# Kernel optimization log

Hardware: AMD Instinct MI355X
Metric: run time of the kernel (lower is better)

The kernel has to match this reference:

```python
import jax, jax.numpy as jnp
import numpy as np

N = 6144          # num utterances (graph nodes)
D = 128           # utt_embed_size
WIN = 10          # att_window_size
NUM_SPK = 8
N_EMO = 7


def _init(key, shape):
    fan_in = shape[0]
    return jax.random.normal(key, shape, dtype=jnp.float32) * (1.0 / np.sqrt(fan_in))


def setup_inputs() -> dict:
    key = jax.random.key(0)
    ks = jax.random.split(key, 20)
    inp = {
        "x": jax.random.normal(ks[0], (N, D), dtype=jnp.float32),
        "speakers": jax.random.randint(ks[1], (N,), 0, NUM_SPK, dtype=jnp.int32),
        # layer-1 relation GCN weights (pred / suc / same / diff)
        "W_pred1": _init(ks[2], (D, D)),
        "W_suc1": _init(ks[3], (D, D)),
        "W_same1": _init(ks[4], (D, D)),
        "W_diff1": _init(ks[5], (D, D)),
        # layer-2 relation GCN weights
        "W_pred2": _init(ks[6], (D, D)),
        "W_suc2": _init(ks[7], (D, D)),
        "W_same2": _init(ks[8], (D, D)),
        "W_diff2": _init(ks[9], (D, D)),
        "w_aggr_1": _init(ks[10], (D, D)),
        "w_aggr_2": _init(ks[11], (D, D)),
        "w_e1": _init(ks[12], (2 * D, D)),
        "b_e1": jnp.zeros((D,), dtype=jnp.float32),
        "w_e2": _init(ks[13], (D, N_EMO)),
        "b_e2": jnp.zeros((N_EMO,), dtype=jnp.float32),
        "w_s": _init(ks[14], (2 * D, N_EMO)),
        "b_s": jnp.zeros((N_EMO,), dtype=jnp.float32),
    }
    return inp


def reference(x, speakers, W_pred1, W_suc1, W_same1, W_diff1,
              W_pred2, W_suc2, W_same2, W_diff2,
              w_aggr_1, w_aggr_2, w_e1, b_e1, w_e2, b_e2, w_s, b_s):
    n = x.shape[0]
    idx = jnp.arange(n)
    # windowed dot-product attention; entries outside the window stay 0.0
    # BEFORE the softmax (faithful to the torch code: zeros, not -inf)
    band = jnp.abs(idx[:, None] - idx[None, :]) <= WIN
    scores = jnp.where(band, x @ x.T, 0.0)            # [N, N]
    attn = jax.nn.softmax(scores, axis=1)
    # relation masks
    same = (speakers[:, None] == speakers[None, :]).astype(x.dtype)
    pred = (idx[None, :] >= idx[:, None]).astype(x.dtype)   # triu incl diag
    suc = 1.0 - pred                                          # strict lower tri
    adjs = (same * pred * attn,        # same-speaker, predecessor
            same * suc * attn,         # same-speaker, successor
            (1.0 - same) * pred * attn,  # diff-speaker, predecessor
            (1.0 - same) * suc * attn)   # diff-speaker, successor

    def gcn(h, Ws):  # sum_k adj_k @ (h @ W_k)
        return sum(a @ (h @ w) for a, w in zip(adjs, Ws))

    d = jnp.diagonal(attn)[:, None]   # self-attention scale
    h1 = jax.nn.relu(gcn(x, (W_pred1, W_suc1, W_same1, W_diff1))
                     + (x @ w_aggr_1) * d)
    h2 = jax.nn.relu(gcn(h1, (W_pred2, W_suc2, W_same2, W_diff2))
                     + (h1 @ w_aggr_2) * d)
    h = jnp.concatenate([h2, x], axis=1)              # [N, 2D]
    emotion = jax.nn.relu(h @ w_e1 + b_e1) @ w_e2 + b_e2   # [N, 7]
    sentiment = h @ w_s + b_s                               # [N, 7]
    return emotion, sentiment
```

## Files before the change

### kernel.cpp

```cpp
#include <hip/hip_runtime.h>
#include <hip/hip_bf16.h>


#define NN   6144
#define DD   128
#define WINW 10
#define YST  168
#define TAB_OFF 27456
#define SS_OFF  33088
#define SM_BYTES 35904
#define NBLK 768
#define WS_W1T 0
#define WS_W2T 163840
#define WS_WE1 327680
#define WS_WE2 393216
#define WS_WST 397312
#define WS_H1  405504
#define WS_H2  1978368
#define BAR_OFF 3551232
#define BAR_STRIDE 16384
#define BAR_BYTES (3 * BAR_STRIDE)

typedef unsigned short u16;
typedef __attribute__((ext_vector_type(8))) short bf16x8;
typedef __attribute__((ext_vector_type(4))) float f32x4;

__device__ __forceinline__ float b2f(u16 u) {
    return __uint_as_float(((unsigned int)u) << 16);
}
__device__ __forceinline__ u16 f2b(float f) {
    __hip_bfloat16 h = __float2bfloat16(f);
    return *reinterpret_cast<u16*>(&h);
}
__device__ __forceinline__ bf16x8 cvt8(const float* p) {
    float4 u = *reinterpret_cast<const float4*>(p);
    float4 v = *reinterpret_cast<const float4*>(p + 4);
    bf16x8 r;
    r[0] = (short)f2b(u.x); r[1] = (short)f2b(u.y);
    r[2] = (short)f2b(u.z); r[3] = (short)f2b(u.w);
    r[4] = (short)f2b(v.x); r[5] = (short)f2b(v.y);
    r[6] = (short)f2b(v.z); r[7] = (short)f2b(v.w);
    return r;
}
__device__ __forceinline__ void st_agent_u32(unsigned* p, unsigned v) {
    __hip_atomic_store(p, v, __ATOMIC_RELAXED, __HIP_MEMORY_SCOPE_AGENT);
}
__device__ __forceinline__ unsigned ld_agent_u32(const unsigned* p) {
    return __hip_atomic_load(p, __ATOMIC_RELAXED, __HIP_MEMORY_SCOPE_AGENT);
}
__device__ __forceinline__ const float* sel5(int r,
    const float* a0, const float* a1, const float* a2,
    const float* a3, const float* a4) {
    return r == 0 ? a0 : r == 1 ? a1 : r == 2 ? a2 : r == 3 ? a3 : a4;
}

__device__ __forceinline__ void grid_barrier(char* barbase, int b) {
    __syncthreads();
    if (threadIdx.x == 0) {
        char* base = barbase + b * BAR_STRIDE;
        unsigned g = blockIdx.x >> 5;
        unsigned* gctr  = (unsigned*)(base + g * 128);
        unsigned* rctr  = (unsigned*)(base + 4096);
        unsigned* gflag = (unsigned*)(base + 8192 + g * 128);
        unsigned* rflag = (unsigned*)(base + 12288);
        unsigned r = __hip_atomic_fetch_add(gctr, 1u, __ATOMIC_RELAXED,
                                            __HIP_MEMORY_SCOPE_AGENT);
        if (r == 31u) {
            unsigned rr = __hip_atomic_fetch_add(rctr, 1u, __ATOMIC_RELAXED,
                                                 __HIP_MEMORY_SCOPE_AGENT);
            if (rr == 23u) {
                st_agent_u32(rflag, 1u);
            } else {
                while (ld_agent_u32(rflag) == 0u)
                    __builtin_amdgcn_s_sleep(1);
            }
            st_agent_u32(gflag, 1u);
        } else {
            while (ld_agent_u32(gflag) == 0u)
                __builtin_amdgcn_s_sleep(1);
        }
    }
    __syncthreads();
    __builtin_amdgcn_sched_barrier(0);
}

__device__ __forceinline__ void layer_tile(
    const float* __restrict__ x, const u16* __restrict__ Ab16,
    const u16* __restrict__ BT, const int* __restrict__ spk,
    u16* __restrict__ hout, int first_layer, int hb, int bm,
    char* smraw, int tid)
{
    u16*   Ys  = (u16*)smraw;
    float* Xs  = (float*)smraw;
    int2*  tab = (int2*)(smraw + TAB_OFF);
    float* Ss  = (float*)(smraw + SS_OFF);
    const int wave = tid >> 6, lane = tid & 63;
    const int lm = lane & 15, quad = lane >> 4;
    const int wm = wave >> 1, wn = wave & 1;

    bf16x8 afr[2][4];

    if (first_layer) {
        #pragma unroll
        for (int it = 0; it < 7; ++it) {
            int f = tid + it * 256;
            if (f < 52 * 32) {
                int s = f >> 5, c = f & 31;
                int g = min(max(bm - WINW + s, 0), NN - 1);
                *reinterpret_cast<float4*>(&Xs[s * 132 + c * 4]) =
                    *reinterpret_cast<const float4*>(&x[(size_t)g * DD + c * 4]);
            }
        }
        __syncthreads();

        #pragma unroll
        for (int rr = 0; rr < 3; ++rr) {
            int p = tid + rr * 256;
            if (p < 672) {
                int il = p / 21, o = p - il * 21;
                int jg = bm + il - WINW + o;
                float sv = -1e30f;
                if (jg >= 0 && jg < NN) {
                    const float* xr = &Xs[(il + WINW) * 132];
                    const float* jr = &Xs[(il + o) * 132];
                    float a0 = 0.f, a1 = 0.f, a2 = 0.f, a3 = 0.f;
                    #pragma unroll 8
                    for (int k4 = 0; k4 < 32; ++k4) {
                        float4 a = *reinterpret_cast<const float4*>(xr + k4 * 4);
                        float4 b = *reinterpret_cast<const float4*>(jr + k4 * 4);
                        a0 = fmaf(a.x, b.x, a0); a1 = fmaf(a.y, b.y, a1);
                        a2 = fmaf(a.z, b.z, a2); a3 = fmaf(a.w, b.w, a3);
                    }
                    sv = (a0 + a1) + (a2 + a3);
                }
                Ss[il * 22 + o] = sv;
            }
        }
        __syncthreads();

        if (tid < 32) {
            int il = tid, i = bm + il;
            float m = 0.f;
            #pragma unroll
            for (int o = 0; o < 21; ++o) {
                float s = Ss[il * 22 + o];
                if (s > -1e29f) m = fmaxf(m, s);
            }
            int lo = i - WINW; if (lo < 0) lo = 0;
            int hi = i + WINW; if (hi > NN - 1) hi = NN - 1;
            float Z = (float)(NN - (hi - lo + 1)) * __expf(-m);
            float ev[21];
            #pragma unroll
            for (int o = 0; o < 21; ++o) {
                float s = Ss[il * 22 + o];
                ev[o] = (s > -1e29f) ? __expf(s - m) : 0.f;
                Z += ev[o];
            }
            float rz = 1.f / Z;
            #pragma unroll
            for (int o = 0; o < 21; ++o) Ss[il * 22 + o] = ev[o] * rz;
        }
        __syncthreads();

        #pragma unroll
        for (int rr = 0; rr < 3; ++rr) {
            int p = tid + rr * 256;
            if (p < 704) {
                int il = p / 22, e = p - il * 22;
                int i  = bm + il;
                int si = spk[i];
                float w; int off;
                if (e < 21) {
                    int j = i - WINW + e;
                    bool valid = (j >= 0) && (j < NN);
                    int jc  = valid ? j : i;
                    int sel = (spk[jc] == si) ? ((j >= i) ? 0 : 1)
                                              : ((j >= i) ? 2 : 3);
                    w   = valid ? Ss[il * 22 + e] : 0.f;
                    off = valid ? (il + e) * YST + sel * 32 : 0;
                } else {
                    w   = Ss[il * 22 + WINW];
                    off = (il + WINW) * YST + 4 * 32;
                }
                tab[p] = make_int2(__float_as_int(w), off);
            }
        }

        #pragma unroll
        for (int mt = 0; mt < 2; ++mt) {
            int rl = min((wm * 2 + mt) * 16 + lm, 51);
            #pragma unroll
            for (int s = 0; s < 4; ++s)
                afr[mt][s] = cvt8(&Xs[rl * 132 + s * 32 + quad * 8]);
        }
        __syncthreads();
    } else {
        #pragma unroll
        for (int mt = 0; mt < 2; ++mt) {
            int gr = min(max(bm - WINW + (wm * 2 + mt) * 16 + lm, 0), NN - 1);
            #pragma unroll
            for (int s = 0; s < 4; ++s)
                afr[mt][s] = *reinterpret_cast<const bf16x8*>(
                    Ab16 + (size_t)gr * DD + s * 32 + quad * 8);
        }
    }

    f32x4 acc[2][5];
    #pragma unroll
    for (int mt = 0; mt < 2; ++mt)
        #pragma unroll
        for (int n = 0; n < 5; ++n) acc[mt][n] = {0.f, 0.f, 0.f, 0.f};

    #pragma unroll
    for (int np = 0; np < 5; ++np) {
        int nt = wn * 5 + np;
        int gn = (nt >> 1) * 128 + hb * 32 + (nt & 1) * 16 + lm;
        #pragma unroll
        for (int s = 0; s < 4; ++s) {
            bf16x8 b = *reinterpret_cast<const bf16x8*>(
                BT + (size_t)gn * DD + s * 32 + quad * 8);
            acc[0][np] = __builtin_amdgcn_mfma_f32_16x16x32_bf16(afr[0][s], b, acc[0][np], 0, 0, 0);
            acc[1][np] = __builtin_amdgcn_mfma_f32_16x16x32_bf16(afr[1][s], b, acc[1][np], 0, 0, 0);
        }
    }
    #pragma unroll
    for (int mt = 0; mt < 2; ++mt)
        #pragma unroll
        for (int np = 0; np < 5; ++np) {
            int nt = wn * 5 + np;
            #pragma unroll
            for (int r = 0; r < 4; ++r) {
                int lr = (wm * 2 + mt) * 16 + quad * 4 + r;
                if (lr < 52) Ys[lr * YST + nt * 16 + lm] = f2b(acc[mt][np][r]);
            }
        }
    __syncthreads();

    const int c0 = (tid & 15) * 2;
    const int rg = tid >> 4;
    #pragma unroll
    for (int rr = 0; rr < 2; ++rr) {
        int il = rg * 2 + rr;
        float a0 = 0.f, a1 = 0.f;
        const int2* tp = &tab[il * 22];
        #pragma unroll
        for (int e = 0; e < 22; ++e) {
            int2 t = tp[e];
            float w = __int_as_float(t.x);
            unsigned y2 = *reinterpret_cast<const unsigned*>(Ys + t.y + c0);
            a0 = fmaf(w, b2f((u16)(y2 & 0xffff)), a0);
            a1 = fmaf(w, b2f((u16)(y2 >> 16)), a1);
        }
        int i = bm + il;
        unsigned pk = ((unsigned)f2b(fmaxf(a1, 0.f)) << 16) | f2b(fmaxf(a0, 0.f));
        st_agent_u32(reinterpret_cast<unsigned*>(
            &hout[(size_t)i * DD + hb * 32 + c0]), pk);
    }
}

__global__ __launch_bounds__(256, 4) void fused_kernel(
    const float* __restrict__ x, const int* __restrict__ spk,
    const float* __restrict__ p0, const float* __restrict__ p1,
    const float* __restrict__ p2, const float* __restrict__ p3,
    const float* __restrict__ p4,
    const float* __restrict__ q0, const float* __restrict__ q1,
    const float* __restrict__ q2, const float* __restrict__ q3,
    const float* __restrict__ q4,
    const float* __restrict__ we1, const float* __restrict__ be1,
    const float* __restrict__ we2, const float* __restrict__ be2,
    const float* __restrict__ wss, const float* __restrict__ bss,
    float* __restrict__ out, char* __restrict__ ws)
{
    u16*   W1T   = (u16*)(ws + WS_W1T);
    u16*   W2T   = (u16*)(ws + WS_W2T);
    u16*   We1T  = (u16*)(ws + WS_WE1);
    u16*   we2T  = (u16*)(ws + WS_WE2);
    u16*   wsT   = (u16*)(ws + WS_WST);
    u16*   h1b   = (u16*)(ws + WS_H1);
    u16*   h2b   = (u16*)(ws + WS_H2);
    char*  bar   = ws + BAR_OFF;

    __shared__ __align__(16) char smraw[SM_BYTES];
    const int bid = blockIdx.x;
    const int tid = threadIdx.x;

    if (bid < 160) {
        unsigned* W1T32 = (unsigned*)W1T;
        unsigned* W2T32 = (unsigned*)W2T;
        int idx = bid * 256 + tid;
        int c = idx & 127, rk = idx >> 7;
        int r = rk >> 6, k2 = rk & 63, k = k2 * 2;
        const float* s1 = sel5(r, p0, p1, p2, p3, p4);
        const float* s2 = sel5(r, q0, q1, q2, q3, q4);
        unsigned v1 = (unsigned)f2b(s1[k * 128 + c]) |
                      ((unsigned)f2b(s1[(k + 1) * 128 + c]) << 16);
        unsigned v2 = (unsigned)f2b(s2[k * 128 + c]) |
                      ((unsigned)f2b(s2[(k + 1) * 128 + c]) << 16);
        int U = (r * 128 + c) * 64 + k2;
        st_agent_u32(&W1T32[U], v1);
        st_agent_u32(&W2T32[U], v2);
    } else if (bid < 192) {
        unsigned* We1T32 = (unsigned*)We1T;
        #pragma unroll
        for (int it = 0; it < 2; ++it) {
            int idx = (bid - 160) * 256 + tid + it * 8192;
            int n = idx & 127, k2 = idx >> 7, k = k2 * 2;
            unsigned v = (unsigned)f2b(we1[k * 128 + n]) |
                         ((unsigned)f2b(we1[(k + 1) * 128 + n]) << 16);
            st_agent_u32(&We1T32[n * 128 + k2], v);
        }
    } else if (bid == 192) {
        unsigned* we2T32 = (unsigned*)we2T;
        #pragma unroll
        for (int it = 0; it < 4; ++it) {
            int U = tid + it * 256;
            int n = U >> 6, kh = U & 63, k = kh * 2;
            float lo = n < 7 ? we2[k * 7 + n] : 0.f;
            float hi = n < 7 ? we2[(k + 1) * 7 + n] : 0.f;
            st_agent_u32(&we2T32[U],
                         (unsigned)f2b(lo) | ((unsigned)f2b(hi) << 16));
        }
    } else if (bid == 193) {
        unsigned* wsT32 = (unsigned*)wsT;
        #pragma unroll
        for (int it = 0; it < 8; ++it) {
            int U = tid + it * 256;
            int n = U >> 7, kh = U & 127, k = kh * 2;
            float lo = n < 7 ? wss[k * 7 + n] : 0.f;
            float hi = n < 7 ? wss[(k + 1) * 7 + n] : 0.f;
            st_agent_u32(&wsT32[U],
                         (unsigned)f2b(lo) | ((unsigned)f2b(hi) << 16));
        }
    }

    grid_barrier(bar, 0);

    const int hb = bid / 192, bmi = bid - hb * 192;
    const int bm = bmi * 32;
    layer_tile(x, nullptr, W1T, spk, h1b, 1, hb, bm, smraw, tid);

    grid_barrier(bar, 1);

    layer_tile(nullptr, h1b, W2T, spk, h2b, 0, hb, bm, smraw, tid);

    grid_barrier(bar, 2);

    if (bid < 384) {
        float* Es = (float*)smraw;
        const int wave = tid >> 6, lane = tid & 63;
        const int lm = lane & 15, quad = lane >> 4;
        const int rt = (bid & ~15) | ((bid & 7) << 1) | ((bid >> 3) & 1);
        const int bmh = rt * 16;
        const int row = bmh + lm;

        bf16x8 afr[8];
        #pragma unroll
        for (int s = 0; s < 4; ++s)
            afr[s] = *reinterpret_cast<const bf16x8*>(
                &h2b[(size_t)row * DD + s * 32 + quad * 8]);
        #pragma unroll
        for (int s = 4; s < 8; ++s)
            afr[s] = cvt8(&x[(size_t)row * DD + (s - 4) * 32 + quad * 8]);

        f32x4 accE[2], accS = {0.f, 0.f, 0.f, 0.f};
        #pragma unroll
        for (int n = 0; n < 2; ++n) accE[n] = {0.f, 0.f, 0.f, 0.f};

        #pragma unroll
        for (int s = 0; s < 8; ++s) {
            #pragma unroll
            for (int n = 0; n < 2; ++n) {
                int nt = wave * 2 + n;
                bf16x8 b = *reinterpret_cast<const bf16x8*>(
                    &We1T[(size_t)(nt * 16 + lm) * 256 + s * 32 + quad * 8]);
                accE[n] = __builtin_amdgcn_mfma_f32_16x16x32_bf16(afr[s], b, accE[n], 0, 0, 0);
            }
            if (wave == 0) {
                bf16x8 bsf = *reinterpret_cast<const bf16x8*>(
                    &wsT[(size_t)lm * 256 + s * 32 + quad * 8]);
                accS = __builtin_amdgcn_mfma_f32_16x16x32_bf16(afr[s], bsf, accS, 0, 0, 0);
            }
        }

        if (wave == 0 && lm < 7) {
            #pragma unroll
            for (int r = 0; r < 4; ++r) {
                int i = bmh + quad * 4 + r;
                out[(size_t)NN * 7 + (size_t)i * 7 + lm] = accS[r] + bss[lm];
            }
        }
        #pragma unroll
        for (int n = 0; n < 2; ++n) {
            int col = (wave * 2 + n) * 16 + lm;
            float bias = be1[col];
            #pragma unroll
            for (int r = 0; r < 4; ++r)
                Es[(quad * 4 + r) * 132 + col] = fmaxf(accE[n][r] + bias, 0.f);
        }
        __syncthreads();

        if (wave == 0) {
            f32x4 accM = {0.f, 0.f, 0.f, 0.f};
            #pragma unroll
            for (int s = 0; s < 4; ++s) {
                bf16x8 a = cvt8(&Es[lm * 132 + s * 32 + quad * 8]);
                bf16x8 b = *reinterpret_cast<const bf16x8*>(
                    &we2T[(size_t)lm * 128 + s * 32 + quad * 8]);
                accM = __builtin_amdgcn_mfma_f32_16x16x32_bf16(a, b, accM, 0, 0, 0);
            }
            if (lm < 7) {
                #pragma unroll
                for (int r = 0; r < 4; ++r) {
                    int i = bmh + quad * 4 + r;
                    out[(size_t)i * 7 + lm] = accM[r] + be2[lm];
                }
            }
        }
    }
}

extern "C" void kernel_launch(void* const* d_in, const int* in_sizes, int n_in,
                              void* d_out, int out_size, void* d_ws, size_t ws_size,
                              hipStream_t stream)
{
    const float* x   = (const float*)d_in[0];
    const int*   spk = (const int*)d_in[1];
    const float* Wp1 = (const float*)d_in[2];
    const float* Wu1 = (const float*)d_in[3];
    const float* Wm1 = (const float*)d_in[4];
    const float* Wd1 = (const float*)d_in[5];
    const float* Wp2 = (const float*)d_in[6];
    const float* Wu2 = (const float*)d_in[7];
    const float* Wm2 = (const float*)d_in[8];
    const float* Wd2 = (const float*)d_in[9];
    const float* wa1 = (const float*)d_in[10];
    const float* wa2 = (const float*)d_in[11];
    const float* we1 = (const float*)d_in[12];
    const float* be1 = (const float*)d_in[13];
    const float* we2 = (const float*)d_in[14];
    const float* be2 = (const float*)d_in[15];
    const float* wss = (const float*)d_in[16];
    const float* bss = (const float*)d_in[17];
    float* out = (float*)d_out;
    char*  ws  = (char*)d_ws;

    hipMemsetAsync(ws + BAR_OFF, 0, BAR_BYTES, stream);

    fused_kernel<<<dim3(NBLK), dim3(256), 0, stream>>>(
        x, spk, Wp1, Wu1, Wm1, Wd1, wa1, Wp2, Wu2, Wm2, Wd2, wa2,
        we1, be1, we2, be2, wss, bss, out, ws);
}
```

Measured before the change: 137.7 us.

## Replace grid barriers with split arrive/wait and per-tile neighbor flags

Drops the full grid barriers between phases. The first barrier becomes split: blocks arrive after weight conversion and only wait after loading and staging their layer-1 input tile. Layer 2 and the head instead wait on per-row-tile counters from the neighbouring tiles, so blocks proceed once their data dependencies are met rather than waiting on the whole grid. This cuts barrier stall and exposes overlap, but the dependency tracking is finer grained and a wrong neighbour range or counter target would race.

```diff
diff --git a/kernel.cpp b/kernel.cpp
--- a/kernel.cpp
+++ b/kernel.cpp
@@ -18,8 +18,9 @@
 #define WS_H1  405504
 #define WS_H2  1978368
 #define BAR_OFF 3551232
-#define BAR_STRIDE 16384
-#define BAR_BYTES (3 * BAR_STRIDE)
+#define F1_OFF 16384
+#define F2_OFF 40960
+#define BAR_BYTES 65536
 
 typedef unsigned short u16;
 typedef __attribute__((ext_vector_type(8))) short bf16x8;
@@ -48,47 +49,24 @@
 __device__ __forceinline__ unsigned ld_agent_u32(const unsigned* p) {
     return __hip_atomic_load(p, __ATOMIC_RELAXED, __HIP_MEMORY_SCOPE_AGENT);
 }
+__device__ __forceinline__ unsigned add_agent_u32(unsigned* p, unsigned v) {
+    return __hip_atomic_fetch_add(p, v, __ATOMIC_RELAXED,
+                                  __HIP_MEMORY_SCOPE_AGENT);
+}
+__device__ __forceinline__ void poll_ge(unsigned* p, unsigned v) {
+    while (ld_agent_u32(p) < v) __builtin_amdgcn_s_sleep(1);
+}
 __device__ __forceinline__ const float* sel5(int r,
     const float* a0, const float* a1, const float* a2,
     const float* a3, const float* a4) {
     return r == 0 ? a0 : r == 1 ? a1 : r == 2 ? a2 : r == 3 ? a3 : a4;
 }
 
-__device__ __forceinline__ void grid_barrier(char* barbase, int b) {
-    __syncthreads();
-    if (threadIdx.x == 0) {
-        char* base = barbase + b * BAR_STRIDE;
-        unsigned g = blockIdx.x >> 5;
-        unsigned* gctr  = (unsigned*)(base + g * 128);
-        unsigned* rctr  = (unsigned*)(base + 4096);
-        unsigned* gflag = (unsigned*)(base + 8192 + g * 128);
-        unsigned* rflag = (unsigned*)(base + 12288);
-        unsigned r = __hip_atomic_fetch_add(gctr, 1u, __ATOMIC_RELAXED,
-                                            __HIP_MEMORY_SCOPE_AGENT);
-        if (r == 31u) {
-            unsigned rr = __hip_atomic_fetch_add(rctr, 1u, __ATOMIC_RELAXED,
-                                                 __HIP_MEMORY_SCOPE_AGENT);
-            if (rr == 23u) {
-                st_agent_u32(rflag, 1u);
-            } else {
-                while (ld_agent_u32(rflag) == 0u)
-                    __builtin_amdgcn_s_sleep(1);
-            }
-            st_agent_u32(gflag, 1u);
-        } else {
-            while (ld_agent_u32(gflag) == 0u)
-                __builtin_amdgcn_s_sleep(1);
-        }
-    }
-    __syncthreads();
-    __builtin_amdgcn_sched_barrier(0);
-}
-
 __device__ __forceinline__ void layer_tile(
     const float* __restrict__ x, const u16* __restrict__ Ab16,
     const u16* __restrict__ BT, const int* __restrict__ spk,
     u16* __restrict__ hout, int first_layer, int hb, int bm,
-    char* smraw, int tid)
+    char* smraw, int tid, char* gate, int bid)
 {
     u16*   Ys  = (u16*)smraw;
     float* Xs  = (float*)smraw;
@@ -194,6 +172,22 @@
                 afr[mt][s] = cvt8(&Xs[rl * 132 + s * 32 + quad * 8]);
         }
         __syncthreads();
+
+        if (gate) {
+            if (tid == 0) {
+                unsigned g = (unsigned)bid >> 5;
+                unsigned* gflag = (unsigned*)(gate + 8192 + g * 128);
+                unsigned* rflag = (unsigned*)(gate + 12288);
+                if ((bid & 31) == 0) {
+                    poll_ge(rflag, 1u);
+                    st_agent_u32(gflag, 1u);
+                } else {
+                    poll_ge(gflag, 1u);
+                }
+            }
+            __syncthreads();
+            __builtin_amdgcn_sched_barrier(0);
+        }
     } else {
         #pragma unroll
         for (int mt = 0; mt < 2; ++mt) {
@@ -279,6 +273,8 @@
     u16*   h1b   = (u16*)(ws + WS_H1);
     u16*   h2b   = (u16*)(ws + WS_H2);
     char*  bar   = ws + BAR_OFF;
+    unsigned* flag1 = (unsigned*)(bar + F1_OFF);
+    unsigned* flag2 = (unsigned*)(bar + F2_OFF);
 
     __shared__ __align__(16) char smraw[SM_BYTES];
     const int bid = blockIdx.x;
@@ -333,24 +329,48 @@
         }
     }
 
-    grid_barrier(bar, 0);
+    __syncthreads();
+    if (tid == 0) {
+        unsigned g = (unsigned)bid >> 5;
+        unsigned* gctr = (unsigned*)(bar + g * 128);
+        unsigned* rctr = (unsigned*)(bar + 4096);
+        unsigned* rflag = (unsigned*)(bar + 12288);
+        unsigned r = add_agent_u32(gctr, 1u);
+        if (r == 31u) {
+            unsigned rr = add_agent_u32(rctr, 1u);
+            if (rr == 23u) st_agent_u32(rflag, 1u);
+        }
+    }
 
     const int hb = bid / 192, bmi = bid - hb * 192;
     const int bm = bmi * 32;
-    layer_tile(x, nullptr, W1T, spk, h1b, 1, hb, bm, smraw, tid);
-
-    grid_barrier(bar, 1);
-
-    layer_tile(nullptr, h1b, W2T, spk, h2b, 0, hb, bm, smraw, tid);
-
-    grid_barrier(bar, 2);
+    layer_tile(x, nullptr, W1T, spk, h1b, 1, hb, bm, smraw, tid, bar, bid);
+
+    __syncthreads();
+    if (tid == 0) add_agent_u32(&flag1[bmi * 32], 1u);
+    if (tid == 0) {
+        if (bmi > 0)   poll_ge(&flag1[(bmi - 1) * 32], 4u);
+        poll_ge(&flag1[bmi * 32], 4u);
+        if (bmi < 191) poll_ge(&flag1[(bmi + 1) * 32], 4u);
+    }
+    __syncthreads();
+    __builtin_amdgcn_sched_barrier(0);
+
+    layer_tile(nullptr, h1b, W2T, spk, h2b, 0, hb, bm, smraw, tid, nullptr, bid);
+
+    __syncthreads();
+    if (tid == 0) add_agent_u32(&flag2[bmi * 32], 1u);
 
     if (bid < 384) {
+        const int rt = (bid & ~15) | ((bid & 7) << 1) | ((bid >> 3) & 1);
+        const int bmh = rt * 16;
+        if (tid == 0) poll_ge(&flag2[(rt >> 1) * 32], 4u);
+        __syncthreads();
+        __builtin_amdgcn_sched_barrier(0);
+
         float* Es = (float*)smraw;
         const int wave = tid >> 6, lane = tid & 63;
         const int lm = lane & 15, quad = lane >> 4;
-        const int rt = (bid & ~15) | ((bid & 7) << 1) | ((bid >> 3) & 1);
-        const int bmh = rt * 16;
         const int row = bmh + lm;
 
         bf16x8 afr[8];
```

After: 131.5 us. 1.05x faster.
